# Kernel tuning notes

Hardware: AMD Instinct MI355X
Metric: run time of the kernel (lower is better)

Reference implementation:

```python
import jax, jax.numpy as jnp
import numpy as np
from jax import lax

EPS = 1e-08


def setup_inputs() -> dict:
    key = jax.random.key(0)
    k1, k2, k3 = jax.random.split(key, 3)
    B, Cin, Cout, K, H, W = 8, 512, 512, 3, 64, 64
    feature_map = jax.random.normal(k1, (B, Cin, H, W), dtype=jnp.float32)
    style = jax.random.normal(k2, (B, Cin), dtype=jnp.float32)
    weight = jax.random.normal(k3, (Cout, Cin, K, K), dtype=jnp.float32)
    return {"feature_map": feature_map, "style": style, "weight": weight}


def reference(feature_map, style, weight):
    # EqualizedWeight: scale raw N(0,1) weight by 1/sqrt(fan_in)
    Cout, Cin, K, _ = weight.shape
    gain = 1.0 / np.sqrt(Cin * K * K)
    w = weight * gain  # (O, I, K, K)

    # Modulate: per-sample scale of input channels -> (B, O, I, K, K)
    w = w[None] * style[:, None, :, None, None]

    # Demodulate: normalize each (b, o) filter to unit norm
    sigma_inv = lax.rsqrt(jnp.sum(w * w, axis=(2, 3, 4), keepdims=True) + EPS)
    w = w * sigma_inv

    # Per-sample conv2d, padding 'same' (equivalent to the groups=B trick)
    def conv_one(x, wi):  # x: (I, H, W), wi: (O, I, K, K)
        return lax.conv_general_dilated(
            x[None], wi, window_strides=(1, 1), padding="SAME",
            dimension_numbers=("NCHW", "OIHW", "NCHW"))[0]

    return jax.vmap(conv_one)(feature_map, w)  # (B, O, H, W)
```

## Files before the change

### kernel.cpp

```cpp
#include <hip/hip_runtime.h>

typedef unsigned short u16;
typedef __attribute__((ext_vector_type(8))) short s16x8;
typedef __attribute__((ext_vector_type(4))) float floatx4;

#define XT_ROWELEMS 2112
#define XT_CGELEMS  139392
#define XT_PB       4460544ull
#define WM_PB       4718592ull

#define GLDS(gp, lp) __builtin_amdgcn_global_load_lds(                      \
    (const __attribute__((address_space(1))) void*)(gp),                    \
    (__attribute__((address_space(3))) void*)(lp), 16, 0, 0)

__device__ __forceinline__ u16 f2bf(float f) {
  union { float f; unsigned u; } x; x.f = f;
  unsigned r = x.u + 0x7fffu + ((x.u >> 16) & 1u);
  return (u16)(r >> 16);
}

__global__ __launch_bounds__(256) void transpose_nchw32(
    const float* __restrict__ fm, u16* __restrict__ xt, int b0)
{
  const int y = blockIdx.x, cg = blockIdx.y, bl = blockIdx.z, tid = threadIdx.x;
  __shared__ float sm[64 * 33];
  const int x = tid & 63, cq = tid >> 6;
  const float* src = fm + (((size_t)(b0 + bl) * 512 + cg * 32) * 64 + y) * 64;
#pragma unroll
  for (int j = 0; j < 8; ++j) {
    int ci = j * 4 + cq;
    sm[x * 33 + ci] = src[(size_t)ci * 4096 + x];
  }

  u16* cgbase = xt + (size_t)(bl * 16 + cg) * XT_CGELEMS;
  const uint4 z = {0u, 0u, 0u, 0u};
  u16* rowb = cgbase + (size_t)(y + 1) * XT_ROWELEMS;
  if (tid < 4)              ((uint4*)rowb)[tid] = z;
  else if (tid < 8)         ((uint4*)(rowb + 65 * 32))[tid - 4] = z;
  if (y == 0)  for (int i = tid; i < 264; i += 256) ((uint4*)cgbase)[i] = z;
  if (y == 63) for (int i = tid; i < 264; i += 256) ((uint4*)(cgbase + 65 * XT_ROWELEMS))[i] = z;

  __syncthreads();
  u16* dst = rowb + 32;
  union { u16 s[8]; uint4 v; } u;
#pragma unroll
  for (int j = 0; j < 8; ++j) {
    int e = tid * 8 + j;
    u.s[j] = f2bf(sm[(e >> 5) * 33 + (e & 31)]);
  }
  ((uint4*)dst)[tid] = u.v;
}

__global__ __launch_bounds__(256) void modulate(
    const float* __restrict__ w, const float* __restrict__ style,
    u16* __restrict__ wm, int b0)
{
  const int o = blockIdx.x, bl = blockIdx.y, tid = threadIdx.x;
  __shared__ float sv[4608];
  __shared__ float red[4];
  const float gain = 0.014731391f;
  const float* wo = w + (size_t)o * 4608;
  const float* st = style + (size_t)(b0 + bl) * 512;
  float ss = 0.f;
#pragma unroll
  for (int j = 0; j < 18; ++j) {
    int idx = j * 256 + tid;
    float v = wo[idx] * gain * st[idx / 9];
    sv[idx] = v;
    ss += v * v;
  }
#pragma unroll
  for (int off = 32; off > 0; off >>= 1) ss += __shfl_down(ss, off, 64);
  if ((tid & 63) == 0) red[tid >> 6] = ss;
  __syncthreads();
  float sinv = rsqrtf(red[0] + red[1] + red[2] + red[3] + 1e-8f);
  const int og = o >> 7, o128 = o & 127;
  u16* base = wm + ((size_t)((bl * 4 + og) * 9) * 16 * 128 + o128) * 32;
#pragma unroll
  for (int j = 0; j < 18; ++j) {
    int e = j * 256 + tid;
    int t = e >> 9, c = e & 511;
    base[((size_t)(t * 16 + (c >> 5))) * 4096 + (c & 31)] = f2bf(sv[c * 9 + t] * sinv);
  }
}

__global__ __launch_bounds__(256, 3) void conv_mfma(
    const u16* __restrict__ Wmod, const u16* __restrict__ xt,
    float* __restrict__ out, int b0, int nb)
{
  const int id = blockIdx.x;
  const int bl = id % nb;
  const int rest = id / nb;
  const int og = rest & 3, p_blk = rest >> 2;
  const int tid = threadIdx.x;
  const int lane = tid & 63, wave = tid >> 6;
  const int wm_off = (wave & 1) * 64, wn_off = (wave >> 1) * 64;
  const int l15 = lane & 15, quad = lane >> 4;

  __shared__ __align__(16) u16 As[2][4096];
  __shared__ __align__(16) u16 Bs[8448];

  const int y0 = p_blk * 2;
  const size_t xt_base = ((size_t)(bl * 16) * XT_CGELEMS) + (size_t)y0 * XT_ROWELEMS;
  const size_t w_base = (size_t)((bl * 4 + og) * 9) * 16 * 4096;

  auto stage_b = [&](int cg) {
    const char* g = (const char*)(xt + xt_base + (size_t)cg * XT_CGELEMS);
    for (int r = wave; r < 16; r += 4)
      GLDS(g + r * 1024 + lane * 16, (char*)Bs + r * 1024);
    if (wave == 0 && lane < 32)
      GLDS(g + 16384 + lane * 16, (char*)Bs + 16384);
  };
  auto stage_a = [&](int t, int cg, int buf) {
    const char* g = (const char*)(Wmod + w_base + (size_t)(t * 16 + cg) * 4096);
    for (int r = wave; r < 8; r += 4)
      GLDS(g + r * 1024 + lane * 16, (char*)As[buf] + r * 1024);
  };

  floatx4 acc[4][4];
  const floatx4 zf = {0.f, 0.f, 0.f, 0.f};
#pragma unroll
  for (int mt = 0; mt < 4; ++mt)
#pragma unroll
    for (int nt = 0; nt < 4; ++nt) acc[mt][nt] = zf;

  stage_b(0);
  stage_a(0, 0, 0);
  __syncthreads();

  for (int cg = 0; cg < 16; ++cg) {
    for (int t = 0; t < 9; ++t) {
      const int cur = (cg * 9 + t) & 1, nxt = cur ^ 1;
      const bool last = (cg == 15 && t == 8);
      const bool cgb = (t == 8 && cg < 15);
      if (!last) stage_a(t < 8 ? t + 1 : 0, t < 8 ? cg : cg + 1, nxt);

      const int ky = t / 3, kx = t - ky * 3;
      s16x8 afr[4], bfr[4];
      const u16* Ab = As[cur];
#pragma unroll
      for (int mt = 0; mt < 4; ++mt)
        afr[mt] = *(const s16x8*)&Ab[(wm_off + mt * 16 + l15) * 32 + quad * 8];
#pragma unroll
      for (int nt = 0; nt < 4; ++nt) {
        int p = wn_off + nt * 16 + l15;
        int r = (p >> 6) + ky, c = (p & 63) + kx;
        bfr[nt] = *(const s16x8*)&Bs[(r * 66 + c) * 32 + quad * 8];
      }
#pragma unroll
      for (int mt = 0; mt < 4; ++mt)
#pragma unroll
        for (int nt = 0; nt < 4; ++nt)
          acc[mt][nt] = __builtin_amdgcn_mfma_f32_16x16x32_bf16(
              afr[mt], bfr[nt], acc[mt][nt], 0, 0, 0);

      if (cgb) {
        __syncthreads();
        stage_b(cg + 1);
      }
      __syncthreads();
    }
  }

  float* outp = out + ((size_t)(b0 + bl) * 512 + og * 128) * 4096 + p_blk * 128;
#pragma unroll
  for (int mt = 0; mt < 4; ++mt)
#pragma unroll
    for (int nt = 0; nt < 4; ++nt) {
      int n = wn_off + nt * 16 + l15;
#pragma unroll
      for (int r = 0; r < 4; ++r) {
        int m = wm_off + mt * 16 + quad * 4 + r;
        outp[(size_t)m * 4096 + n] = acc[mt][nt][r];
      }
    }
}

__global__ __launch_bounds__(256) void conv_direct(
    const float* __restrict__ fm, const float* __restrict__ style,
    const float* __restrict__ w, float* __restrict__ out)
{
  const int o = blockIdx.x, b = blockIdx.y, tid = threadIdx.x;
  __shared__ float swm[4608];
  __shared__ float red[4];
  const float gain = 0.014731391f;
  const float* wo = w + (size_t)o * 4608;
  const float* st = style + (size_t)b * 512;
  float ss = 0.f;
#pragma unroll
  for (int j = 0; j < 18; ++j) {
    int idx = j * 256 + tid;
    float v = wo[idx] * gain * st[idx / 9];
    swm[idx] = v;
    ss += v * v;
  }
#pragma unroll
  for (int off = 32; off > 0; off >>= 1) ss += __shfl_down(ss, off, 64);
  if ((tid & 63) == 0) red[tid >> 6] = ss;
  __syncthreads();
  const float sinv = rsqrtf(red[0] + red[1] + red[2] + red[3] + 1e-8f);

  const int y = tid >> 2, x0 = (tid & 3) * 16;
  float acc[16];
#pragma unroll
  for (int i = 0; i < 16; ++i) acc[i] = 0.f;
  const float* fb = fm + (size_t)b * 512 * 4096;
  for (int ci = 0; ci < 512; ++ci) {
    const float* fc = fb + (size_t)ci * 4096;
    const float* wr = swm + ci * 9;
#pragma unroll
    for (int ky = 0; ky < 3; ++ky) {
      int yy = y + ky - 1;
      if (yy < 0 || yy > 63) continue;
      const float* frow = fc + yy * 64;
#pragma unroll
      for (int kx = 0; kx < 3; ++kx) {
        float wv = wr[ky * 3 + kx];
#pragma unroll
        for (int i = 0; i < 16; ++i) {
          int xx = x0 + i + kx - 1;
          float xv = (xx >= 0 && xx < 64) ? frow[xx] : 0.f;
          acc[i] += wv * xv;
        }
      }
    }
  }
  float* op = out + ((size_t)b * 512 + o) * 4096 + y * 64 + x0;
#pragma unroll
  for (int i = 0; i < 16; ++i) op[i] = acc[i] * sinv;
}

extern "C" void kernel_launch(void* const* d_in, const int* in_sizes, int n_in,
                              void* d_out, int out_size, void* d_ws, size_t ws_size,
                              hipStream_t stream) {
  const float* fm = (const float*)d_in[0];
  const float* style = (const float*)d_in[1];
  const float* w = (const float*)d_in[2];
  float* out = (float*)d_out;

  if (ws_size < XT_PB + WM_PB) {
    conv_direct<<<dim3(512, 8), 256, 0, stream>>>(fm, style, w, out);
    return;
  }
  int nb = 8;
  while (nb > 1 && (size_t)nb * (XT_PB + WM_PB) > ws_size) nb >>= 1;

  u16* xt = (u16*)d_ws;
  u16* wmod = (u16*)((char*)d_ws + (size_t)nb * XT_PB);

  for (int b0 = 0; b0 < 8; b0 += nb) {
    transpose_nchw32<<<dim3(64, 16, nb), 256, 0, stream>>>(fm, xt, b0);
    modulate<<<dim3(512, nb), 256, 0, stream>>>(w, style, wmod, b0);
    conv_mfma<<<dim3(32 * 4 * nb), 256, 0, stream>>>(wmod, xt, out, b0, nb);
  }
}
```

Before: 325.3 us.

## Swizzle LDS layouts and deepen weight prefetch pipeline with manual waitcnt barriers

The transpose and modulate kernels now write their bf16 outputs with an XOR-swizzled 16-byte slot order, and the conv kernel reads A and B fragments with the matching swizzle to cut LDS bank conflicts. The A-tile buffer grows from two to four stages with prefetch three steps ahead. Per-step __syncthreads are replaced by explicit s_waitcnt vmcnt plus s_barrier, with setprio around the MFMA block. Address math is hoisted and the tap loop fully unrolled, which costs more LDS and code size and depends on the hand-tuned wait counts being correct.

```diff
diff --git a/kernel.cpp b/kernel.cpp
--- a/kernel.cpp
+++ b/kernel.cpp
@@ -12,6 +12,9 @@
 #define GLDS(gp, lp) __builtin_amdgcn_global_load_lds(                      \
     (const __attribute__((address_space(1))) void*)(gp),                    \
     (__attribute__((address_space(3))) void*)(lp), 16, 0, 0)
+
+#define WAITVM(N) asm volatile("s_waitcnt vmcnt(" #N ")" ::: "memory")
+#define SBAR()    asm volatile("s_barrier" ::: "memory")
 
 __device__ __forceinline__ u16 f2bf(float f) {
   union { float f; unsigned u; } x; x.f = f;
@@ -41,14 +44,15 @@
   if (y == 63) for (int i = tid; i < 264; i += 256) ((uint4*)(cgbase + 65 * XT_ROWELEMS))[i] = z;
 
   __syncthreads();
-  u16* dst = rowb + 32;
   union { u16 s[8]; uint4 v; } u;
 #pragma unroll
   for (int j = 0; j < 8; ++j) {
     int e = tid * 8 + j;
     u.s[j] = f2bf(sm[(e >> 5) * 33 + (e & 31)]);
   }
-  ((uint4*)dst)[tid] = u.v;
+  const int col = 1 + (tid >> 2);
+  const int slot = (tid & 3) ^ ((col >> 1) & 3);
+  ((uint4*)rowb)[col * 4 + slot] = u.v;
 }
 
 __global__ __launch_bounds__(256) void modulate(
@@ -75,12 +79,13 @@
   __syncthreads();
   float sinv = rsqrtf(red[0] + red[1] + red[2] + red[3] + 1e-8f);
   const int og = o >> 7, o128 = o & 127;
+  const int axor = ((o128 >> 1) & 3) << 3;
   u16* base = wm + ((size_t)((bl * 4 + og) * 9) * 16 * 128 + o128) * 32;
 #pragma unroll
   for (int j = 0; j < 18; ++j) {
     int e = j * 256 + tid;
     int t = e >> 9, c = e & 511;
-    base[((size_t)(t * 16 + (c >> 5))) * 4096 + (c & 31)] = f2bf(sv[c * 9 + t] * sinv);
+    base[((size_t)(t * 16 + (c >> 5))) * 4096 + ((c & 31) ^ axor)] = f2bf(sv[c * 9 + t] * sinv);
   }
 }
 
@@ -97,7 +102,7 @@
   const int wm_off = (wave & 1) * 64, wn_off = (wave >> 1) * 64;
   const int l15 = lane & 15, quad = lane >> 4;
 
-  __shared__ __align__(16) u16 As[2][4096];
+  __shared__ __align__(16) u16 As[4][4096];
   __shared__ __align__(16) u16 Bs[8448];
 
   const int y0 = p_blk * 2;
@@ -117,6 +122,19 @@
       GLDS(g + r * 1024 + lane * 16, (char*)As[buf] + r * 1024);
   };
 
+  int aoff[4];
+#pragma unroll
+  for (int mt = 0; mt < 4; ++mt) {
+    int row = wm_off + mt * 16 + l15;
+    aoff[mt] = row * 32 + ((quad ^ ((row >> 1) & 3)) << 3);
+  }
+  int pr[4], pc[4];
+#pragma unroll
+  for (int nt = 0; nt < 4; ++nt) {
+    int p = wn_off + nt * 16 + l15;
+    pr[nt] = p >> 6; pc[nt] = p & 63;
+  }
+
   floatx4 acc[4][4];
   const floatx4 zf = {0.f, 0.f, 0.f, 0.f};
 #pragma unroll
@@ -126,39 +144,52 @@
 
   stage_b(0);
   stage_a(0, 0, 0);
-  __syncthreads();
-
+  stage_a(1, 0, 1);
+  stage_a(2, 0, 2);
+  __syncthreads();
+
+#pragma unroll 1
   for (int cg = 0; cg < 16; ++cg) {
+#pragma unroll
     for (int t = 0; t < 9; ++t) {
-      const int cur = (cg * 9 + t) & 1, nxt = cur ^ 1;
-      const bool last = (cg == 15 && t == 8);
-      const bool cgb = (t == 8 && cg < 15);
-      if (!last) stage_a(t < 8 ? t + 1 : 0, t < 8 ? cg : cg + 1, nxt);
+      const int s = cg * 9 + t;
+      const int cur = s & 3;
+      if (t == 0)         WAITVM(0);
+      else if (s <= 141)  WAITVM(2);
+      else if (s == 142)  WAITVM(1);
+      else                WAITVM(0);
+      SBAR();
+      if (s + 3 < 144) {
+        int t3 = t + 3, cg3 = cg;
+        if (t3 >= 9) { t3 -= 9; ++cg3; }
+        stage_a(t3, cg3, (s + 3) & 3);
+      }
 
       const int ky = t / 3, kx = t - ky * 3;
       s16x8 afr[4], bfr[4];
       const u16* Ab = As[cur];
 #pragma unroll
       for (int mt = 0; mt < 4; ++mt)
-        afr[mt] = *(const s16x8*)&Ab[(wm_off + mt * 16 + l15) * 32 + quad * 8];
+        afr[mt] = *(const s16x8*)&Ab[aoff[mt]];
 #pragma unroll
       for (int nt = 0; nt < 4; ++nt) {
-        int p = wn_off + nt * 16 + l15;
-        int r = (p >> 6) + ky, c = (p & 63) + kx;
-        bfr[nt] = *(const s16x8*)&Bs[(r * 66 + c) * 32 + quad * 8];
-      }
+        int r = pr[nt] + ky, c = pc[nt] + kx;
+        bfr[nt] = *(const s16x8*)&Bs[(r * 66 + c) * 32 + ((quad ^ ((c >> 1) & 3)) << 3)];
+      }
+      __builtin_amdgcn_s_setprio(1);
 #pragma unroll
       for (int mt = 0; mt < 4; ++mt)
 #pragma unroll
         for (int nt = 0; nt < 4; ++nt)
           acc[mt][nt] = __builtin_amdgcn_mfma_f32_16x16x32_bf16(
               afr[mt], bfr[nt], acc[mt][nt], 0, 0, 0);
-
-      if (cgb) {
-        __syncthreads();
+      __builtin_amdgcn_s_setprio(0);
+
+      if (t == 8 && cg < 15) {
+        asm volatile("s_waitcnt lgkmcnt(0)" ::: "memory");
+        SBAR();
         stage_b(cg + 1);
       }
-      __syncthreads();
     }
   }
 
```

Result: slower. 354.1 us (+8.9%).

## Enlarge conv tile to 256 output channels and XOR-swizzle LDS layouts

Applied to the files above, without the earlier changes.

The MFMA conv block now covers 256 output channels instead of 128, so each wave holds an 8x4 accumulator tile. This halves the number of blocks and the re-staging of input tiles per output channel. The modulate and transpose kernels write weights and activations in an XOR-swizzled layout, and the conv kernel reads with a matching swizzle to avoid LDS bank conflicts. The cost is more registers and LDS per block (occupancy hint drops from 3 to 2), and only 512 blocks are launched, which may underfill the GPU.

```diff
diff --git a/kernel.cpp b/kernel.cpp
--- a/kernel.cpp
+++ b/kernel.cpp
@@ -7,6 +7,7 @@
 #define XT_ROWELEMS 2112
 #define XT_CGELEMS  139392
 #define XT_PB       4460544ull
+#define WM_ELEMS    2359296ull
 #define WM_PB       4718592ull
 
 #define GLDS(gp, lp) __builtin_amdgcn_global_load_lds(                      \
@@ -41,14 +42,15 @@
   if (y == 63) for (int i = tid; i < 264; i += 256) ((uint4*)(cgbase + 65 * XT_ROWELEMS))[i] = z;
 
   __syncthreads();
-  u16* dst = rowb + 32;
   union { u16 s[8]; uint4 v; } u;
 #pragma unroll
   for (int j = 0; j < 8; ++j) {
     int e = tid * 8 + j;
     u.s[j] = f2bf(sm[(e >> 5) * 33 + (e & 31)]);
   }
-  ((uint4*)dst)[tid] = u.v;
+  const int col = 1 + (tid >> 2);
+  const int slot = (tid & 3) ^ ((col >> 1) & 3);
+  ((uint4*)rowb)[col * 4 + slot] = u.v;
 }
 
 __global__ __launch_bounds__(256) void modulate(
@@ -74,35 +76,35 @@
   if ((tid & 63) == 0) red[tid >> 6] = ss;
   __syncthreads();
   float sinv = rsqrtf(red[0] + red[1] + red[2] + red[3] + 1e-8f);
-  const int og = o >> 7, o128 = o & 127;
-  u16* base = wm + ((size_t)((bl * 4 + og) * 9) * 16 * 128 + o128) * 32;
+  const int axor = ((o >> 1) & 3) << 3;
+  u16* base = wm + (size_t)bl * WM_ELEMS + (size_t)o * 32;
 #pragma unroll
   for (int j = 0; j < 18; ++j) {
     int e = j * 256 + tid;
     int t = e >> 9, c = e & 511;
-    base[((size_t)(t * 16 + (c >> 5))) * 4096 + (c & 31)] = f2bf(sv[c * 9 + t] * sinv);
-  }
-}
-
-__global__ __launch_bounds__(256, 3) void conv_mfma(
+    base[((size_t)(t * 16 + (c >> 5))) * 16384 + ((c & 31) ^ axor)] = f2bf(sv[c * 9 + t] * sinv);
+  }
+}
+
+__global__ __launch_bounds__(256, 2) void conv_mfma(
     const u16* __restrict__ Wmod, const u16* __restrict__ xt,
     float* __restrict__ out, int b0, int nb)
 {
   const int id = blockIdx.x;
   const int bl = id % nb;
   const int rest = id / nb;
-  const int og = rest & 3, p_blk = rest >> 2;
+  const int og = rest & 1, p_blk = rest >> 1;
   const int tid = threadIdx.x;
   const int lane = tid & 63, wave = tid >> 6;
-  const int wm_off = (wave & 1) * 64, wn_off = (wave >> 1) * 64;
+  const int wm_off = (wave & 1) * 128, wn_off = (wave >> 1) * 64;
   const int l15 = lane & 15, quad = lane >> 4;
 
-  __shared__ __align__(16) u16 As[2][4096];
+  __shared__ __align__(16) u16 As[2][8192];
   __shared__ __align__(16) u16 Bs[8448];
 
   const int y0 = p_blk * 2;
   const size_t xt_base = ((size_t)(bl * 16) * XT_CGELEMS) + (size_t)y0 * XT_ROWELEMS;
-  const size_t w_base = (size_t)((bl * 4 + og) * 9) * 16 * 4096;
+  const size_t w_base = (size_t)bl * WM_ELEMS + (size_t)og * (256 * 32);
 
   auto stage_b = [&](int cg) {
     const char* g = (const char*)(xt + xt_base + (size_t)cg * XT_CGELEMS);
@@ -112,15 +114,28 @@
       GLDS(g + 16384 + lane * 16, (char*)Bs + 16384);
   };
   auto stage_a = [&](int t, int cg, int buf) {
-    const char* g = (const char*)(Wmod + w_base + (size_t)(t * 16 + cg) * 4096);
-    for (int r = wave; r < 8; r += 4)
+    const char* g = (const char*)(Wmod + w_base + (size_t)(t * 16 + cg) * 16384);
+    for (int r = wave; r < 16; r += 4)
       GLDS(g + r * 1024 + lane * 16, (char*)As[buf] + r * 1024);
   };
 
-  floatx4 acc[4][4];
+  int aoff[8];
+#pragma unroll
+  for (int mt = 0; mt < 8; ++mt) {
+    int row = wm_off + mt * 16 + l15;
+    aoff[mt] = row * 32 + ((quad ^ ((row >> 1) & 3)) << 3);
+  }
+  int pr[4], pc[4];
+#pragma unroll
+  for (int nt = 0; nt < 4; ++nt) {
+    int p = wn_off + nt * 16 + l15;
+    pr[nt] = p >> 6; pc[nt] = p & 63;
+  }
+
+  floatx4 acc[8][4];
   const floatx4 zf = {0.f, 0.f, 0.f, 0.f};
 #pragma unroll
-  for (int mt = 0; mt < 4; ++mt)
+  for (int mt = 0; mt < 8; ++mt)
 #pragma unroll
     for (int nt = 0; nt < 4; ++nt) acc[mt][nt] = zf;
 
@@ -128,7 +143,9 @@
   stage_a(0, 0, 0);
   __syncthreads();
 
+#pragma unroll 1
   for (int cg = 0; cg < 16; ++cg) {
+#pragma unroll 1
     for (int t = 0; t < 9; ++t) {
       const int cur = (cg * 9 + t) & 1, nxt = cur ^ 1;
       const bool last = (cg == 15 && t == 8);
@@ -136,19 +153,18 @@
       if (!last) stage_a(t < 8 ? t + 1 : 0, t < 8 ? cg : cg + 1, nxt);
 
       const int ky = t / 3, kx = t - ky * 3;
-      s16x8 afr[4], bfr[4];
+      s16x8 afr[8], bfr[4];
       const u16* Ab = As[cur];
 #pragma unroll
-      for (int mt = 0; mt < 4; ++mt)
-        afr[mt] = *(const s16x8*)&Ab[(wm_off + mt * 16 + l15) * 32 + quad * 8];
-#pragma unroll
       for (int nt = 0; nt < 4; ++nt) {
-        int p = wn_off + nt * 16 + l15;
-        int r = (p >> 6) + ky, c = (p & 63) + kx;
-        bfr[nt] = *(const s16x8*)&Bs[(r * 66 + c) * 32 + quad * 8];
-      }
-#pragma unroll
-      for (int mt = 0; mt < 4; ++mt)
+        int r = pr[nt] + ky, c = pc[nt] + kx;
+        bfr[nt] = *(const s16x8*)&Bs[(r * 66 + c) * 32 + ((quad ^ ((c >> 1) & 3)) << 3)];
+      }
+#pragma unroll
+      for (int mt = 0; mt < 8; ++mt)
+        afr[mt] = *(const s16x8*)&Ab[aoff[mt]];
+#pragma unroll
+      for (int mt = 0; mt < 8; ++mt)
 #pragma unroll
         for (int nt = 0; nt < 4; ++nt)
           acc[mt][nt] = __builtin_amdgcn_mfma_f32_16x16x32_bf16(
@@ -162,9 +178,9 @@
     }
   }
 
-  float* outp = out + ((size_t)(b0 + bl) * 512 + og * 128) * 4096 + p_blk * 128;
-#pragma unroll
-  for (int mt = 0; mt < 4; ++mt)
+  float* outp = out + ((size_t)(b0 + bl) * 512 + og * 256) * 4096 + p_blk * 128;
+#pragma unroll
+  for (int mt = 0; mt < 8; ++mt)
 #pragma unroll
     for (int nt = 0; nt < 4; ++nt) {
       int n = wn_off + nt * 16 + l15;
@@ -251,6 +267,6 @@
   for (int b0 = 0; b0 < 8; b0 += nb) {
     transpose_nchw32<<<dim3(64, 16, nb), 256, 0, stream>>>(fm, xt, b0);
     modulate<<<dim3(512, nb), 256, 0, stream>>>(w, style, wmod, b0);
-    conv_mfma<<<dim3(32 * 4 * nb), 256, 0, stream>>>(wmod, xt, out, b0, nb);
-  }
-}
+    conv_mfma<<<dim3(64 * nb), 256, 0, stream>>>(wmod, xt, out, b0, nb);
+  }
+}
```

Measured after the change: 274.5 us. 1.19x faster.
